# Kernel optimization log

Measured on AMD Instinct MI355X. Metric: run time of the kernel, lower is better.

The kernel has to match this reference:

```python
import jax, jax.numpy as jnp
import numpy as np

DILATIONS = (1, 2, 4, 8, 16, 32, 64, 128, 256, 512)
K = 3            # kernel_size
CH = 128         # channels
B, T = 4, 16384
L = len(DILATIONS)


def _conv1x1(x, w, b=None):
    # x: [B, Cin, T], w: [Cout, Cin, 1] -> [B, Cout, T]
    y = jnp.einsum('oc,bct->bot', w[..., 0], x)
    return y if b is None else y + b[None, :, None]


def _causal_dilated_conv(x, w, b, d):
    # buffer of zeros of size (K-1)*d concatenated on the left == causal left pad
    pad = (K - 1) * d
    y = jax.lax.conv_general_dilated(
        x, w, window_strides=(1,), padding=[(pad, 0)], rhs_dilation=(d,),
        dimension_numbers=('NCH', 'OIH', 'NCH'))
    return y + b[None, :, None]


def setup_inputs() -> dict:
    key = jax.random.key(0)
    ks = jax.random.split(key, 12)
    s = 0.1  # keep gated activations out of saturation
    return {
        'x': jax.random.normal(ks[0], (B, 1, T), jnp.float32),
        'c': jax.random.normal(ks[1], (B, 1, T), jnp.float32),
        'head_init': jnp.zeros((B, CH, T), jnp.float32),
        'w_re': jax.random.normal(ks[2], (CH, 1, 1), jnp.float32) * s,
        'conv_w': jax.random.normal(ks[3], (L, 2 * CH, CH, K), jnp.float32) * s,
        'conv_b': jax.random.normal(ks[4], (L, 2 * CH), jnp.float32) * s,
        'mix_w': jax.random.normal(ks[5], (L, 2 * CH, 1, 1), jnp.float32) * s,
        'w1x1': jax.random.normal(ks[6], (L, CH, CH, 1), jnp.float32) * s,
        'b1x1': jax.random.normal(ks[7], (L, CH), jnp.float32) * s,
        'w_head': jax.random.normal(ks[8], (1, CH, 1), jnp.float32) * s,
        'b_head': jax.random.normal(ks[9], (1,), jnp.float32) * s,
    }


def reference(x, c, head_init, w_re, conv_w, conv_b, mix_w, w1x1, b1x1, w_head, b_head):
    h = _conv1x1(x, w_re)               # rechannel: [B, CH, T]
    head = head_init                    # head accumulator (zeros == head_input=None)
    for li, d in enumerate(DILATIONS):  # fixed small layer loop (structurally distinct dilations)
        z = _causal_dilated_conv(h, conv_w[li], conv_b[li], d)   # [B, 2CH, T]
        z = z + _conv1x1(c, mix_w[li])                           # conditioning mixer
        post = jnp.tanh(z[:, :CH]) * jax.nn.sigmoid(z[:, CH:])   # gated activation
        h = h + _conv1x1(post, w1x1[li], b1x1[li])               # residual
        head = head + post
    out = _conv1x1(head, w_head, b_head)  # [B, 1, T]
    return out, h
```

## Files before the change

### kernel.cpp

```cpp
#include <hip/hip_runtime.h>
#include <hip/hip_bf16.h>

#define B_   4
#define T_   16384
#define CH_  128
#define TCH_ 256
#define NL_  10
#define TT_  64
#define SHW_ 196

typedef __attribute__((ext_vector_type(8))) short short8;
typedef __attribute__((ext_vector_type(4))) float f32x4;

#define MFMA16(a, b, c) __builtin_amdgcn_mfma_f32_16x16x32_bf16(a, b, c, 0, 0, 0)

__device__ __forceinline__ unsigned short f2bf(float f) {
  unsigned u = __float_as_uint(f);
  return (unsigned short)((u + 0x7FFFu + ((u >> 16) & 1u)) >> 16);
}
__device__ __forceinline__ unsigned pk2bf(float lo, float hi) {
  unsigned r;
  asm("v_cvt_pk_bf16_f32 %0, %1, %2" : "=v"(r) : "v"(lo), "v"(hi));
  return r;
}
__device__ __forceinline__ float bf2f(unsigned s) {
  return __uint_as_float((s & 0xFFFFu) << 16);
}
__device__ __forceinline__ float fast_tanh(float x) {
  float e = __expf(2.0f * fabsf(x));
  float t = 1.0f - 2.0f / (e + 1.0f);
  return copysignf(t, x);
}
__device__ __forceinline__ float fast_sig(float x) {
  return 1.0f / (1.0f + __expf(-x));
}

__global__ __launch_bounds__(256) void pack_w(
    const float* __restrict__ conv_w, const float* __restrict__ w1x1,
    unsigned short* __restrict__ wpackA, unsigned short* __restrict__ wpack1) {
  const int NA = NL_ * 4 * 4 * 12 * 64 * 8;
  int idx = blockIdx.x * 256 + threadIdx.x;
  if (idx < NA) {
    int j = idx & 7;
    int t1 = idx >> 3;
    int l = t1 & 63;
    int t2 = t1 >> 6;
    int ks = t2 % 12;
    int t3 = t2 / 12;
    int f = t3 & 3;
    int t4 = t3 >> 2;
    int w = t4 & 3;
    int li = t4 >> 2;
    int o = 32 * w + 16 * (f & 1) + 128 * (f >> 1) + (l & 15);
    int ck = 32 * ks + 8 * (l >> 4) + j;
    int c = ck & 127, k = ck >> 7;
    wpackA[idx] = f2bf(conv_w[((li * TCH_ + o) * CH_ + c) * 3 + k]);
  } else {
    int i2 = idx - NA;
    if (i2 < NL_ * 4 * 2 * 4 * 64 * 8) {
      int j = i2 & 7;
      int t1 = i2 >> 3;
      int l = t1 & 63;
      int t2 = t1 >> 6;
      int ks = t2 & 3;
      int t3 = t2 >> 2;
      int p = t3 & 1;
      int t4 = t3 >> 1;
      int w = t4 & 3;
      int li = t4 >> 2;
      int o = 32 * w + 16 * p + (l & 15);
      int c = 32 * ks + 8 * (l >> 4) + j;
      wpack1[i2] = f2bf(w1x1[(li * CH_ + o) * CH_ + c]);
    }
  }
}

__global__ __launch_bounds__(256) void rechannel_k(
    const float* __restrict__ x, const float* __restrict__ w_re,
    unsigned short* __restrict__ hb) {
  int flat = blockIdx.x * 256 + threadIdx.x;
  int cid = flat & 15;
  int t = (flat >> 4) & (T_ - 1);
  int b = flat >> 18;
  float xv = x[b * T_ + t];
  const float* wr = w_re + cid * 8;
  union { short8 s; unsigned short u[8]; } o;
#pragma unroll
  for (int j = 0; j < 8; ++j) o.u[j] = f2bf(wr[j] * xv);
  *(short8*)(hb + (size_t)(b * T_ + t) * CH_ + cid * 8) = o.s;
}

__global__ __launch_bounds__(256) void out_init_k(
    const float* __restrict__ head_init, const float* __restrict__ w_head,
    const float* __restrict__ b_head, float* __restrict__ out) {
  int idx = blockIdx.x * 256 + threadIdx.x;
  int b = idx / T_;
  int t = idx - b * T_;
  float acc = b_head[0];
#pragma unroll 8
  for (int c = 0; c < CH_; ++c)
    acc += w_head[c] * head_init[(b * CH_ + c) * T_ + t];
  out[idx] = acc;
}

__global__ __launch_bounds__(512, 6) void layer_k(
    const unsigned short* __restrict__ hin,
    unsigned short* __restrict__ hob,
    float* __restrict__ hof,
    const float* __restrict__ cin, float* __restrict__ out,
    const unsigned short* __restrict__ wA,
    const unsigned short* __restrict__ w1p,
    const float* __restrict__ bconv,
    const float* __restrict__ wmix,
    const float* __restrict__ b1,
    const float* __restrict__ w_head,
    int d, int is_final) {
  __shared__ unsigned shH[TT_ * SHW_];
  __shared__ float shR[8 * 4 * 16];

  const int tid = threadIdx.x;
  const int b = blockIdx.y;
  const int t0 = blockIdx.x * TT_;

#pragma unroll
  for (int it = 0; it < 6; ++it) {
    int flat = it * 512 + tid;
    int cid = flat & 15;
    int tt = (flat >> 4) & 63;
    int k = flat >> 10;
    int t = t0 + tt - (2 - k) * d;
    uint4 v = make_uint4(0u, 0u, 0u, 0u);
    if (t >= 0)
      v = *(const uint4*)(hin + ((size_t)(b * T_ + t) * CH_ + cid * 8));
    *(uint4*)(shH + tt * SHW_ + k * 64 + cid * 4) = v;
  }
  __syncthreads();

  const int wave = __builtin_amdgcn_readfirstlane(tid >> 6);
  const int lane = tid & 63;
  const int r = lane & 15;
  const int g = lane >> 4;
  const int wlo = (wave >> 1) * 4 + (wave & 1);

  f32x4 accLo[4], accHi[4];
#pragma unroll
  for (int q = 0; q < 4; ++q) {
    accLo[q] = (f32x4){0.f, 0.f, 0.f, 0.f};
    accHi[q] = (f32x4){0.f, 0.f, 0.f, 0.f};
  }

  const short8* wAv = (const short8*)wA;
#pragma unroll
  for (int ks = 0; ks < 12; ++ks) {
    short8 bf[4];
#pragma unroll
    for (int q = 0; q < 4; ++q)
      bf[q] = *(const short8*)(shH + (16 * q + r) * SHW_ + 16 * ks + 4 * g);
    short8 alo = wAv[(wlo * 12 + ks) * 64 + lane];
    short8 ahi = wAv[((wlo + 2) * 12 + ks) * 64 + lane];
#pragma unroll
    for (int q = 0; q < 4; ++q) {
      accLo[q] = MFMA16(alo, bf[q], accLo[q]);
      accHi[q] = MFMA16(ahi, bf[q], accHi[q]);
    }
  }
  __syncthreads();

  float bcL[4], bcH[4], wmL[4], wmH[4], whv[4];
#pragma unroll
  for (int j = 0; j < 4; ++j) {
    int o = 16 * wave + 4 * g + j;
    bcL[j] = bconv[o];
    bcH[j] = bconv[o + CH_];
    wmL[j] = wmix[o];
    wmH[j] = wmix[o + CH_];
    whv[j] = w_head[o];
  }

  float hs[4];
#pragma unroll
  for (int q = 0; q < 4; ++q) {
    float cq = cin[b * T_ + t0 + 16 * q + r];
    float pv[4];
#pragma unroll
    for (int j = 0; j < 4; ++j) {
      float zl = accLo[q][j] + bcL[j] + wmL[j] * cq;
      float zh = accHi[q][j] + bcH[j] + wmH[j] * cq;
      pv[j] = fast_tanh(zl) * fast_sig(zh);
    }
    hs[q] = whv[0] * pv[0] + whv[1] * pv[1] + whv[2] * pv[2] + whv[3] * pv[3];
    uint2 pk;
    pk.x = pk2bf(pv[0], pv[1]);
    pk.y = pk2bf(pv[2], pv[3]);
    *(uint2*)(shH + (16 * q + r) * SHW_ + 8 * wave + 2 * g) = pk;
  }
  __syncthreads();

  f32x4 acc2[4];
#pragma unroll
  for (int q = 0; q < 4; ++q) acc2[q] = (f32x4){0.f, 0.f, 0.f, 0.f};

  const short8* w1v = (const short8*)w1p;
#pragma unroll
  for (int ks = 0; ks < 4; ++ks) {
    short8 bp[4];
#pragma unroll
    for (int q = 0; q < 4; ++q)
      bp[q] = *(const short8*)(shH + (16 * q + r) * SHW_ + 16 * ks + 4 * g);
    short8 a1 = w1v[(wave * 4 + ks) * 64 + lane];
#pragma unroll
    for (int q = 0; q < 4; ++q) acc2[q] = MFMA16(a1, bp[q], acc2[q]);
  }

  float res[4][4];
  float b1v[4];
#pragma unroll
  for (int j = 0; j < 4; ++j) b1v[j] = b1[16 * wave + 4 * g + j];
#pragma unroll
  for (int q = 0; q < 4; ++q) {
    uint2 hv = *(const uint2*)(shH + (16 * q + r) * SHW_ + 128 + 8 * wave + 2 * g);
    res[q][0] = bf2f(hv.x) + b1v[0] + acc2[q][0];
    res[q][1] = bf2f(hv.x >> 16) + b1v[1] + acc2[q][1];
    res[q][2] = bf2f(hv.y) + b1v[2] + acc2[q][2];
    res[q][3] = bf2f(hv.y >> 16) + b1v[3] + acc2[q][3];
  }

#pragma unroll
  for (int q = 0; q < 4; ++q) {
    hs[q] += __shfl_xor(hs[q], 16);
    hs[q] += __shfl_xor(hs[q], 32);
  }
  if (g == 0) {
#pragma unroll
    for (int q = 0; q < 4; ++q) shR[(wave * 4 + q) * 16 + r] = hs[q];
  }
  __syncthreads();

  if (tid < 64) {
    int q = tid >> 4, rr = tid & 15;
    float tot = 0.f;
#pragma unroll
    for (int w = 0; w < 8; ++w) tot += shR[(w * 4 + q) * 16 + rr];
    out[b * T_ + t0 + 16 * q + rr] += tot;
  }

  if (!is_final) {
#pragma unroll
    for (int q = 0; q < 4; ++q) {
      uint2 pk;
      pk.x = pk2bf(res[q][0], res[q][1]);
      pk.y = pk2bf(res[q][2], res[q][3]);
      *(uint2*)(shH + (16 * q + r) * SHW_ + 8 * wave + 2 * g) = pk;
    }
    __syncthreads();
#pragma unroll
    for (int it = 0; it < 2; ++it) {
      int flat = it * 512 + tid;
      int cid = flat & 15;
      int tt = flat >> 4;
      *(uint4*)(hob + ((size_t)(b * T_ + t0 + tt) * CH_ + cid * 8)) =
          *(const uint4*)(shH + tt * SHW_ + cid * 4);
    }
  } else {
#pragma unroll
    for (int q = 0; q < 4; ++q) {
#pragma unroll
      for (int j = 0; j < 4; ++j)
        hof[(size_t)(b * CH_ + 16 * wave + 4 * g + j) * T_ + t0 + 16 * q + r] =
            res[q][j];
    }
  }
}

extern "C" void kernel_launch(void* const* d_in, const int* in_sizes, int n_in,
                              void* d_out, int out_size, void* d_ws, size_t ws_size,
                              hipStream_t stream) {
  const float* x         = (const float*)d_in[0];
  const float* c         = (const float*)d_in[1];
  const float* head_init = (const float*)d_in[2];
  const float* w_re      = (const float*)d_in[3];
  const float* conv_w    = (const float*)d_in[4];
  const float* conv_b    = (const float*)d_in[5];
  const float* mix_w     = (const float*)d_in[6];
  const float* w1x1      = (const float*)d_in[7];
  const float* b1x1      = (const float*)d_in[8];
  const float* w_head    = (const float*)d_in[9];
  const float* b_head    = (const float*)d_in[10];

  float* out = (float*)d_out;
  float* hof = out + B_ * T_;

  unsigned short* hb0 = (unsigned short*)d_ws;
  unsigned short* hb1 = hb0 + (size_t)B_ * T_ * CH_;
  unsigned short* wpackA = hb1 + (size_t)B_ * T_ * CH_;
  unsigned short* wpack1 = wpackA + NL_ * 4 * 4 * 12 * 64 * 8;

  const int n_pack = NL_ * 4 * 4 * 12 * 64 * 8 + NL_ * 4 * 2 * 4 * 64 * 8;
  pack_w<<<(n_pack + 255) / 256, 256, 0, stream>>>(conv_w, w1x1, wpackA, wpack1);

  rechannel_k<<<(B_ * T_ * 16) / 256, 256, 0, stream>>>(x, w_re, hb0);
  out_init_k<<<(B_ * T_) / 256, 256, 0, stream>>>(head_init, w_head, b_head, out);

  const int dil[NL_] = {1, 2, 4, 8, 16, 32, 64, 128, 256, 512};
  for (int li = 0; li < NL_; ++li) {
    const unsigned short* hin = (li & 1) ? hb1 : hb0;
    unsigned short* hob       = (li & 1) ? hb0 : hb1;
    int is_final = (li == NL_ - 1);
    layer_k<<<dim3(T_ / TT_, B_), 512, 0, stream>>>(
        hin, hob, hof, c, out,
        wpackA + li * (4 * 4 * 12 * 64 * 8),
        wpack1 + li * (4 * 2 * 4 * 64 * 8),
        conv_b + li * TCH_,
        mix_w + li * TCH_,
        b1x1 + li * CH_,
        w_head,
        dil[li], is_final);
  }
}
```

Measured before the change: 326.8 us.

## Switch layer kernel to 32x32x16 MFMA with 256-thread blocks

```diff
diff --git a/kernel.cpp b/kernel.cpp
--- a/kernel.cpp
+++ b/kernel.cpp
@@ -10,9 +10,9 @@
 #define SHW_ 196
 
 typedef __attribute__((ext_vector_type(8))) short short8;
-typedef __attribute__((ext_vector_type(4))) float f32x4;
-
-#define MFMA16(a, b, c) __builtin_amdgcn_mfma_f32_16x16x32_bf16(a, b, c, 0, 0, 0)
+typedef __attribute__((ext_vector_type(16))) float f32x16;
+
+#define MFMA32(a, b, c) __builtin_amdgcn_mfma_f32_32x32x16_bf16(a, b, c, 0, 0, 0)
 
 __device__ __forceinline__ unsigned short f2bf(float f) {
   unsigned u = __float_as_uint(f);
@@ -38,38 +38,30 @@
 __global__ __launch_bounds__(256) void pack_w(
     const float* __restrict__ conv_w, const float* __restrict__ w1x1,
     unsigned short* __restrict__ wpackA, unsigned short* __restrict__ wpack1) {
-  const int NA = NL_ * 4 * 4 * 12 * 64 * 8;
+  const int NA = NL_ * 8 * 24 * 64 * 8;
   int idx = blockIdx.x * 256 + threadIdx.x;
   if (idx < NA) {
     int j = idx & 7;
-    int t1 = idx >> 3;
-    int l = t1 & 63;
-    int t2 = t1 >> 6;
-    int ks = t2 % 12;
-    int t3 = t2 / 12;
-    int f = t3 & 3;
-    int t4 = t3 >> 2;
-    int w = t4 & 3;
-    int li = t4 >> 2;
-    int o = 32 * w + 16 * (f & 1) + 128 * (f >> 1) + (l & 15);
-    int ck = 32 * ks + 8 * (l >> 4) + j;
-    int c = ck & 127, k = ck >> 7;
-    wpackA[idx] = f2bf(conv_w[((li * TCH_ + o) * CH_ + c) * 3 + k]);
+    int l = (idx >> 3) & 63;
+    int t2 = idx >> 9;
+    int ks = t2 % 24;
+    int t3 = t2 / 24;
+    int of = t3 & 7;
+    int li = t3 >> 3;
+    int o = 32 * of + (l & 31);
+    int ck = 16 * ks + 8 * (l >> 5) + j;
+    int c = ck & 127, ktap = ck >> 7;
+    wpackA[idx] = f2bf(conv_w[((li * TCH_ + o) * CH_ + c) * 3 + ktap]);
   } else {
     int i2 = idx - NA;
-    if (i2 < NL_ * 4 * 2 * 4 * 64 * 8) {
+    if (i2 < NL_ * 4 * 8 * 64 * 8) {
       int j = i2 & 7;
-      int t1 = i2 >> 3;
-      int l = t1 & 63;
-      int t2 = t1 >> 6;
-      int ks = t2 & 3;
-      int t3 = t2 >> 2;
-      int p = t3 & 1;
-      int t4 = t3 >> 1;
-      int w = t4 & 3;
-      int li = t4 >> 2;
-      int o = 32 * w + 16 * p + (l & 15);
-      int c = 32 * ks + 8 * (l >> 4) + j;
+      int l = (i2 >> 3) & 63;
+      int ks = (i2 >> 9) & 7;
+      int of = (i2 >> 12) & 3;
+      int li = i2 >> 14;
+      int o = 32 * of + (l & 31);
+      int c = 16 * ks + 8 * (l >> 5) + j;
       wpack1[i2] = f2bf(w1x1[(li * CH_ + o) * CH_ + c]);
     }
   }
@@ -103,7 +95,7 @@
   out[idx] = acc;
 }
 
-__global__ __launch_bounds__(512, 6) void layer_k(
+__global__ __launch_bounds__(256, 3) void layer_k(
     const unsigned short* __restrict__ hin,
     unsigned short* __restrict__ hob,
     float* __restrict__ hof,
@@ -116,15 +108,16 @@
     const float* __restrict__ w_head,
     int d, int is_final) {
   __shared__ unsigned shH[TT_ * SHW_];
-  __shared__ float shR[8 * 4 * 16];
+  __shared__ float shR[4 * 64];
 
   const int tid = threadIdx.x;
   const int b = blockIdx.y;
-  const int t0 = blockIdx.x * TT_;
-
-#pragma unroll
-  for (int it = 0; it < 6; ++it) {
-    int flat = it * 512 + tid;
+  const int tile = (blockIdx.x & 7) * 32 + (blockIdx.x >> 3);
+  const int t0 = tile * TT_;
+
+#pragma unroll
+  for (int it = 0; it < 12; ++it) {
+    int flat = it * 256 + tid;
     int cid = flat & 15;
     int tt = (flat >> 4) & 63;
     int k = flat >> 10;
@@ -138,124 +131,124 @@
 
   const int wave = __builtin_amdgcn_readfirstlane(tid >> 6);
   const int lane = tid & 63;
-  const int r = lane & 15;
-  const int g = lane >> 4;
-  const int wlo = (wave >> 1) * 4 + (wave & 1);
-
-  f32x4 accLo[4], accHi[4];
-#pragma unroll
-  for (int q = 0; q < 4; ++q) {
-    accLo[q] = (f32x4){0.f, 0.f, 0.f, 0.f};
-    accHi[q] = (f32x4){0.f, 0.f, 0.f, 0.f};
-  }
+  const int ln = lane & 31;
+  const int kg = lane >> 5;
+
+  f32x16 aL0, aL1, aH0, aH1;
+#pragma unroll
+  for (int i = 0; i < 16; ++i) { aL0[i] = 0.f; aL1[i] = 0.f; aH0[i] = 0.f; aH1[i] = 0.f; }
 
   const short8* wAv = (const short8*)wA;
 #pragma unroll
-  for (int ks = 0; ks < 12; ++ks) {
-    short8 bf[4];
-#pragma unroll
-    for (int q = 0; q < 4; ++q)
-      bf[q] = *(const short8*)(shH + (16 * q + r) * SHW_ + 16 * ks + 4 * g);
-    short8 alo = wAv[(wlo * 12 + ks) * 64 + lane];
-    short8 ahi = wAv[((wlo + 2) * 12 + ks) * 64 + lane];
-#pragma unroll
-    for (int q = 0; q < 4; ++q) {
-      accLo[q] = MFMA16(alo, bf[q], accLo[q]);
-      accHi[q] = MFMA16(ahi, bf[q], accHi[q]);
-    }
+  for (int ks = 0; ks < 24; ++ks) {
+    short8 b0 = *(const short8*)(shH + ln * SHW_ + 8 * ks + 4 * kg);
+    short8 b1f = *(const short8*)(shH + (32 + ln) * SHW_ + 8 * ks + 4 * kg);
+    short8 alo = wAv[(wave * 24 + ks) * 64 + lane];
+    short8 ahi = wAv[((wave + 4) * 24 + ks) * 64 + lane];
+    aL0 = MFMA32(alo, b0, aL0);
+    aL1 = MFMA32(alo, b1f, aL1);
+    aH0 = MFMA32(ahi, b0, aH0);
+    aH1 = MFMA32(ahi, b1f, aH1);
   }
   __syncthreads();
 
-  float bcL[4], bcH[4], wmL[4], wmH[4], whv[4];
-#pragma unroll
-  for (int j = 0; j < 4; ++j) {
-    int o = 16 * wave + 4 * g + j;
-    bcL[j] = bconv[o];
-    bcH[j] = bconv[o + CH_];
-    wmL[j] = wmix[o];
-    wmH[j] = wmix[o + CH_];
-    whv[j] = w_head[o];
-  }
-
-  float hs[4];
-#pragma unroll
-  for (int q = 0; q < 4; ++q) {
-    float cq = cin[b * T_ + t0 + 16 * q + r];
-    float pv[4];
-#pragma unroll
-    for (int j = 0; j < 4; ++j) {
-      float zl = accLo[q][j] + bcL[j] + wmL[j] * cq;
-      float zh = accHi[q][j] + bcH[j] + wmH[j] * cq;
-      pv[j] = fast_tanh(zl) * fast_sig(zh);
-    }
-    hs[q] = whv[0] * pv[0] + whv[1] * pv[1] + whv[2] * pv[2] + whv[3] * pv[3];
+  const float cq0 = cin[b * T_ + t0 + ln];
+  const float cq1 = cin[b * T_ + t0 + 32 + ln];
+  float hs0 = 0.f, hs1 = 0.f;
+#pragma unroll
+  for (int r2 = 0; r2 < 4; ++r2) {
+    const int o4 = 32 * wave + 8 * r2 + 4 * kg;
+    const float4 bcL = *(const float4*)(bconv + o4);
+    const float4 bcH = *(const float4*)(bconv + CH_ + o4);
+    const float4 wmL = *(const float4*)(wmix + o4);
+    const float4 wmH = *(const float4*)(wmix + CH_ + o4);
+    const float4 wh = *(const float4*)(w_head + o4);
+    float pv0[4], pv1[4];
+#pragma unroll
+    for (int j2 = 0; j2 < 4; ++j2) {
+      const float bl = ((const float*)&bcL)[j2], bh = ((const float*)&bcH)[j2];
+      const float ml = ((const float*)&wmL)[j2], mh = ((const float*)&wmH)[j2];
+      const float w = ((const float*)&wh)[j2];
+      float zl0 = aL0[4 * r2 + j2] + bl + ml * cq0;
+      float zh0 = aH0[4 * r2 + j2] + bh + mh * cq0;
+      pv0[j2] = fast_tanh(zl0) * fast_sig(zh0);
+      hs0 += w * pv0[j2];
+      float zl1 = aL1[4 * r2 + j2] + bl + ml * cq1;
+      float zh1 = aH1[4 * r2 + j2] + bh + mh * cq1;
+      pv1[j2] = fast_tanh(zl1) * fast_sig(zh1);
+      hs1 += w * pv1[j2];
+    }
     uint2 pk;
-    pk.x = pk2bf(pv[0], pv[1]);
-    pk.y = pk2bf(pv[2], pv[3]);
-    *(uint2*)(shH + (16 * q + r) * SHW_ + 8 * wave + 2 * g) = pk;
+    const int dw = 16 * wave + 4 * r2 + 2 * kg;
+    pk.x = pk2bf(pv0[0], pv0[1]);
+    pk.y = pk2bf(pv0[2], pv0[3]);
+    *(uint2*)(shH + ln * SHW_ + dw) = pk;
+    pk.x = pk2bf(pv1[0], pv1[1]);
+    pk.y = pk2bf(pv1[2], pv1[3]);
+    *(uint2*)(shH + (32 + ln) * SHW_ + dw) = pk;
+  }
+  hs0 += __shfl_xor(hs0, 32);
+  hs1 += __shfl_xor(hs1, 32);
+  if (lane < 32) {
+    shR[wave * 64 + ln] = hs0;
+    shR[wave * 64 + 32 + ln] = hs1;
   }
   __syncthreads();
 
-  f32x4 acc2[4];
-#pragma unroll
-  for (int q = 0; q < 4; ++q) acc2[q] = (f32x4){0.f, 0.f, 0.f, 0.f};
+  f32x16 d0, d1;
+#pragma unroll
+  for (int i = 0; i < 16; ++i) { d0[i] = 0.f; d1[i] = 0.f; }
 
   const short8* w1v = (const short8*)w1p;
 #pragma unroll
-  for (int ks = 0; ks < 4; ++ks) {
-    short8 bp[4];
-#pragma unroll
-    for (int q = 0; q < 4; ++q)
-      bp[q] = *(const short8*)(shH + (16 * q + r) * SHW_ + 16 * ks + 4 * g);
-    short8 a1 = w1v[(wave * 4 + ks) * 64 + lane];
-#pragma unroll
-    for (int q = 0; q < 4; ++q) acc2[q] = MFMA16(a1, bp[q], acc2[q]);
-  }
-
-  float res[4][4];
-  float b1v[4];
-#pragma unroll
-  for (int j = 0; j < 4; ++j) b1v[j] = b1[16 * wave + 4 * g + j];
-#pragma unroll
-  for (int q = 0; q < 4; ++q) {
-    uint2 hv = *(const uint2*)(shH + (16 * q + r) * SHW_ + 128 + 8 * wave + 2 * g);
-    res[q][0] = bf2f(hv.x) + b1v[0] + acc2[q][0];
-    res[q][1] = bf2f(hv.x >> 16) + b1v[1] + acc2[q][1];
-    res[q][2] = bf2f(hv.y) + b1v[2] + acc2[q][2];
-    res[q][3] = bf2f(hv.y >> 16) + b1v[3] + acc2[q][3];
-  }
-
-#pragma unroll
-  for (int q = 0; q < 4; ++q) {
-    hs[q] += __shfl_xor(hs[q], 16);
-    hs[q] += __shfl_xor(hs[q], 32);
-  }
-  if (g == 0) {
-#pragma unroll
-    for (int q = 0; q < 4; ++q) shR[(wave * 4 + q) * 16 + r] = hs[q];
-  }
-  __syncthreads();
+  for (int ks = 0; ks < 8; ++ks) {
+    short8 p0 = *(const short8*)(shH + ln * SHW_ + 8 * ks + 4 * kg);
+    short8 p1 = *(const short8*)(shH + (32 + ln) * SHW_ + 8 * ks + 4 * kg);
+    short8 a = w1v[(wave * 8 + ks) * 64 + lane];
+    d0 = MFMA32(a, p0, d0);
+    d1 = MFMA32(a, p1, d1);
+  }
 
   if (tid < 64) {
-    int q = tid >> 4, rr = tid & 15;
-    float tot = 0.f;
-#pragma unroll
-    for (int w = 0; w < 8; ++w) tot += shR[(w * 4 + q) * 16 + rr];
-    out[b * T_ + t0 + 16 * q + rr] += tot;
+    float tot = shR[tid] + shR[64 + tid] + shR[128 + tid] + shR[192 + tid];
+    out[b * T_ + t0 + tid] += tot;
+  }
+
+  float res0[16], res1[16];
+#pragma unroll
+  for (int r2 = 0; r2 < 4; ++r2) {
+    const int o4 = 32 * wave + 8 * r2 + 4 * kg;
+    const float4 b14 = *(const float4*)(b1 + o4);
+    const int dw = 16 * wave + 4 * r2 + 2 * kg;
+    uint2 h0 = *(const uint2*)(shH + ln * SHW_ + 128 + dw);
+    uint2 h1 = *(const uint2*)(shH + (32 + ln) * SHW_ + 128 + dw);
+    res0[4 * r2 + 0] = bf2f(h0.x) + ((const float*)&b14)[0] + d0[4 * r2 + 0];
+    res0[4 * r2 + 1] = bf2f(h0.x >> 16) + ((const float*)&b14)[1] + d0[4 * r2 + 1];
+    res0[4 * r2 + 2] = bf2f(h0.y) + ((const float*)&b14)[2] + d0[4 * r2 + 2];
+    res0[4 * r2 + 3] = bf2f(h0.y >> 16) + ((const float*)&b14)[3] + d0[4 * r2 + 3];
+    res1[4 * r2 + 0] = bf2f(h1.x) + ((const float*)&b14)[0] + d1[4 * r2 + 0];
+    res1[4 * r2 + 1] = bf2f(h1.x >> 16) + ((const float*)&b14)[1] + d1[4 * r2 + 1];
+    res1[4 * r2 + 2] = bf2f(h1.y) + ((const float*)&b14)[2] + d1[4 * r2 + 2];
+    res1[4 * r2 + 3] = bf2f(h1.y >> 16) + ((const float*)&b14)[3] + d1[4 * r2 + 3];
   }
 
   if (!is_final) {
-#pragma unroll
-    for (int q = 0; q < 4; ++q) {
+    __syncthreads();
+#pragma unroll
+    for (int r2 = 0; r2 < 4; ++r2) {
+      const int dw = 16 * wave + 4 * r2 + 2 * kg;
       uint2 pk;
-      pk.x = pk2bf(res[q][0], res[q][1]);
-      pk.y = pk2bf(res[q][2], res[q][3]);
-      *(uint2*)(shH + (16 * q + r) * SHW_ + 8 * wave + 2 * g) = pk;
+      pk.x = pk2bf(res0[4 * r2 + 0], res0[4 * r2 + 1]);
+      pk.y = pk2bf(res0[4 * r2 + 2], res0[4 * r2 + 3]);
+      *(uint2*)(shH + ln * SHW_ + dw) = pk;
+      pk.x = pk2bf(res1[4 * r2 + 0], res1[4 * r2 + 1]);
+      pk.y = pk2bf(res1[4 * r2 + 2], res1[4 * r2 + 3]);
+      *(uint2*)(shH + (32 + ln) * SHW_ + dw) = pk;
     }
     __syncthreads();
 #pragma unroll
-    for (int it = 0; it < 2; ++it) {
-      int flat = it * 512 + tid;
+    for (int it = 0; it < 4; ++it) {
+      int flat = it * 256 + tid;
       int cid = flat & 15;
       int tt = flat >> 4;
       *(uint4*)(hob + ((size_t)(b * T_ + t0 + tt) * CH_ + cid * 8)) =
@@ -263,11 +256,13 @@
     }
   } else {
 #pragma unroll
-    for (int q = 0; q < 4; ++q) {
-#pragma unroll
-      for (int j = 0; j < 4; ++j)
-        hof[(size_t)(b * CH_ + 16 * wave + 4 * g + j) * T_ + t0 + 16 * q + r] =
-            res[q][j];
+    for (int r2 = 0; r2 < 4; ++r2) {
+#pragma unroll
+      for (int j2 = 0; j2 < 4; ++j2) {
+        const int o = 32 * wave + 8 * r2 + 4 * kg + j2;
+        hof[(size_t)(b * CH_ + o) * T_ + t0 + ln] = res0[4 * r2 + j2];
+        hof[(size_t)(b * CH_ + o) * T_ + t0 + 32 + ln] = res1[4 * r2 + j2];
+      }
     }
   }
 }
@@ -293,9 +288,9 @@
   unsigned short* hb0 = (unsigned short*)d_ws;
   unsigned short* hb1 = hb0 + (size_t)B_ * T_ * CH_;
   unsigned short* wpackA = hb1 + (size_t)B_ * T_ * CH_;
-  unsigned short* wpack1 = wpackA + NL_ * 4 * 4 * 12 * 64 * 8;
-
-  const int n_pack = NL_ * 4 * 4 * 12 * 64 * 8 + NL_ * 4 * 2 * 4 * 64 * 8;
+  unsigned short* wpack1 = wpackA + NL_ * 8 * 24 * 64 * 8;
+
+  const int n_pack = NL_ * 8 * 24 * 64 * 8 + NL_ * 4 * 8 * 64 * 8;
   pack_w<<<(n_pack + 255) / 256, 256, 0, stream>>>(conv_w, w1x1, wpackA, wpack1);
 
   rechannel_k<<<(B_ * T_ * 16) / 256, 256, 0, stream>>>(x, w_re, hb0);
@@ -306,10 +301,10 @@
     const unsigned short* hin = (li & 1) ? hb1 : hb0;
     unsigned short* hob       = (li & 1) ? hb0 : hb1;
     int is_final = (li == NL_ - 1);
-    layer_k<<<dim3(T_ / TT_, B_), 512, 0, stream>>>(
+    layer_k<<<dim3(T_ / TT_, B_), 256, 0, stream>>>(
         hin, hob, hof, c, out,
-        wpackA + li * (4 * 4 * 12 * 64 * 8),
-        wpack1 + li * (4 * 2 * 4 * 64 * 8),
+        wpackA + li * (8 * 24 * 64 * 8),
+        wpack1 + li * (4 * 8 * 64 * 8),
         conv_b + li * TCH_,
         mix_w + li * TCH_,
         b1x1 + li * CH_,
```

Result: faster. 310.8 us (-4.9%).
